# Kernel optimization log

Hardware: AMD Instinct MI355X
Metric: run time of the kernel (lower is better)

The kernel has to match this reference:

```python
import jax, jax.numpy as jnp
import numpy as np
import math

B, T, C, H = 2, 2048, 1024, 16
HD = C // H  # head dim = 64

def setup_inputs() -> dict:
    key = jax.random.key(0)
    ks = jax.random.split(key, 5)
    s = 1.0 / math.sqrt(C)
    return {
        "x": jax.random.normal(ks[0], (B, T, C), jnp.float32),
        "Wq": jax.random.normal(ks[1], (C, C), jnp.float32) * s,
        "bq": jnp.zeros((C,), jnp.float32),
        "Wk": jax.random.normal(ks[2], (C, C), jnp.float32) * s,
        "bk": jnp.zeros((C,), jnp.float32),
        "Wv": jax.random.normal(ks[3], (C, C), jnp.float32) * s,
        "bv": jnp.zeros((C,), jnp.float32),
        "Wp": jax.random.normal(ks[4], (C, C), jnp.float32) * s,
        "bp": jnp.zeros((C,), jnp.float32),
    }

def reference(x, Wq, bq, Wk, bk, Wv, bv, Wp, bp):
    # project and split heads: [B,T,C] -> [B,H,T,HD]
    def heads(y):
        return y.reshape(B, T, H, HD).transpose(0, 2, 1, 3)
    q = heads(x @ Wq + bq)
    k = heads(x @ Wk + bk)
    v = heads(x @ Wv + bv)
    scale = 1.0 / math.sqrt(HD)
    att = jnp.einsum('bhqd,bhkd->bhqk', q, k) * scale  # [B,H,T,T]
    causal = jnp.tril(jnp.ones((T, T), bool))
    att = jnp.where(causal, att, -jnp.inf)
    att = jax.nn.softmax(att, axis=-1)  # attention_dropout p=0 -> identity
    y = jnp.einsum('bhqk,bhkd->bhqd', att, v)  # [B,H,T,HD]
    y = y.transpose(0, 2, 1, 3).reshape(B, T, C)
    return y @ Wp + bp  # residual_dropout p=0 -> identity
```

## Files before the change

kernel.cpp:

```cpp
#include <hip/hip_runtime.h>
#include <hip/hip_bf16.h>
#include <stdint.h>

typedef __bf16 bf16x8 __attribute__((ext_vector_type(8)));
typedef __bf16 bf16x4 __attribute__((ext_vector_type(4)));
typedef float  f32x4  __attribute__((ext_vector_type(4)));

#define MFMA16(a, b, c) __builtin_amdgcn_mfma_f32_16x16x32_bf16(a, b, c, 0, 0, 0)

#if __has_builtin(__builtin_amdgcn_exp2f)
#define EXP2(x) __builtin_amdgcn_exp2f(x)
#else
#define EXP2(x) exp2f(x)
#endif

__device__ __forceinline__ void ld16(void* lds, const void* g) {
    __builtin_amdgcn_global_load_lds(
        (const __attribute__((address_space(1))) void*)(uintptr_t)g,
        (__attribute__((address_space(3))) void*)(uint32_t)(uintptr_t)lds,
        16, 0, 0);
}

__global__ __launch_bounds__(1024) void prep_kernel(const float* __restrict__ x,
                                                    const float* __restrict__ W0,
                                                    const float* __restrict__ W1,
                                                    const float* __restrict__ W2,
                                                    const float* __restrict__ W3,
                                                    __bf16* __restrict__ wdst,
                                                    __bf16* __restrict__ xdst) {
    __shared__ __bf16 t[32][33];
    const int z = blockIdx.z;
    const int tx = threadIdx.x, ty = threadIdx.y;
    if (z == 4) {
        int blin = blockIdx.y * 32 + blockIdx.x;
        int i = (blin * 1024 + ty * 32 + tx) * 4;
        float4 v = *(const float4*)(x + i);
        xdst[i]     = (__bf16)v.x;
        xdst[i + 1] = (__bf16)v.y;
        xdst[i + 2] = (__bf16)v.z;
        xdst[i + 3] = (__bf16)v.w;
        return;
    }
    const float* W = (z == 0) ? W0 : (z == 1) ? W1 : (z == 2) ? W2 : W3;
    __bf16* D = wdst + (size_t)z * 1048576;
    t[ty][tx] = (__bf16)W[(size_t)(blockIdx.y * 32 + ty) * 1024 + blockIdx.x * 32 + tx];
    __syncthreads();
    D[(size_t)(blockIdx.x * 32 + ty) * 1024 + blockIdx.y * 32 + tx] = t[tx][ty];
}

__device__ __forceinline__ void gemm_mainloop(const __bf16* __restrict__ A,
                                              const __bf16* __restrict__ BT,
                                              int K, __bf16* As, __bf16* Bs,
                                              f32x4 acc[4][4]) {
    const int tid  = threadIdx.x;
    const int lane = tid & 63;
    const int wid  = tid >> 6;
    const int quad = lane >> 4;
    const int l16  = lane & 15;
    const int wm   = wid >> 1;
    const int wn   = wid & 1;

    const int srow = wid * 16 + (lane >> 2);
    const int scol = (lane & 3) * 8;
    const int sdst = wid * 512 + lane * 8;

    auto stage = [&](int b, int k0) {
        ld16(As + b * 4096 + sdst,        A  + (size_t)srow        * K + k0 + scol);
        ld16(As + b * 4096 + 2048 + sdst, A  + (size_t)(srow + 64) * K + k0 + scol);
        ld16(Bs + b * 4096 + sdst,        BT + (size_t)srow        * K + k0 + scol);
        ld16(Bs + b * 4096 + 2048 + sdst, BT + (size_t)(srow + 64) * K + k0 + scol);
    };

    stage(0, 0);
    __syncthreads();
    int buf = 0;

    for (int k0 = 0; k0 < K; k0 += 32) {
        if (k0 + 32 < K) stage(buf ^ 1, k0 + 32);
        bf16x8 af[4], bf[4];
#pragma unroll
        for (int mt = 0; mt < 4; mt++)
            af[mt] = *(const bf16x8*)(As + buf * 4096 +
                                      (wm * 64 + mt * 16 + l16) * 32 + quad * 8);
#pragma unroll
        for (int nt = 0; nt < 4; nt++)
            bf[nt] = *(const bf16x8*)(Bs + buf * 4096 +
                                      (wn * 64 + nt * 16 + l16) * 32 + quad * 8);
#pragma unroll
        for (int mt = 0; mt < 4; mt++)
#pragma unroll
            for (int nt = 0; nt < 4; nt++)
                acc[mt][nt] = MFMA16(af[mt], bf[nt], acc[mt][nt]);
        __syncthreads();
        buf ^= 1;
    }
}

__device__ __forceinline__ void mainloop64(const __bf16* __restrict__ A,
                                           const __bf16* __restrict__ BT,
                                           int K, __bf16* As, __bf16* Bs,
                                           f32x4 acc[2][4]) {
    const int tid  = threadIdx.x;
    const int lane = tid & 63;
    const int quad = lane >> 4;
    const int l16  = lane & 15;
    const int wid  = tid >> 6;
    const int wm   = wid >> 1;
    const int wn   = wid & 1;
    const int srow = tid >> 2;
    const int scol = (tid & 3) * 8;

    auto stage = [&](int b, int k0) {
        ld16(As + b * 2048 + tid * 8,        A  + (size_t)srow        * K + k0 + scol);
        ld16(Bs + b * 4096 + tid * 8,        BT + (size_t)srow        * K + k0 + scol);
        ld16(Bs + b * 4096 + 2048 + tid * 8, BT + (size_t)(srow + 64) * K + k0 + scol);
    };

    stage(0, 0);
    __syncthreads();
    int buf = 0;

    for (int k0 = 0; k0 < K; k0 += 32) {
        if (k0 + 32 < K) stage(buf ^ 1, k0 + 32);
        bf16x8 af[2], bf[4];
#pragma unroll
        for (int mt = 0; mt < 2; mt++)
            af[mt] = *(const bf16x8*)(As + buf * 2048 +
                                      (wm * 32 + mt * 16 + l16) * 32 + quad * 8);
#pragma unroll
        for (int nt = 0; nt < 4; nt++)
            bf[nt] = *(const bf16x8*)(Bs + buf * 4096 +
                                      (wn * 64 + nt * 16 + l16) * 32 + quad * 8);
#pragma unroll
        for (int mt = 0; mt < 2; mt++)
#pragma unroll
            for (int nt = 0; nt < 4; nt++)
                acc[mt][nt] = MFMA16(af[mt], bf[nt], acc[mt][nt]);
        __syncthreads();
        buf ^= 1;
    }
}

__global__ __launch_bounds__(256) void qkv_gemm(const __bf16* __restrict__ X,
                                                const __bf16* __restrict__ WTb,
                                                const float* __restrict__ b0,
                                                const float* __restrict__ b1,
                                                const float* __restrict__ b2,
                                                __bf16* __restrict__ qk,
                                                __bf16* __restrict__ vt) {
    __shared__ __attribute__((aligned(16))) __bf16 As[8192];
    __shared__ __attribute__((aligned(16))) __bf16 Bs[8192];
    const int o  = blockIdx.x;
    const int g  = o & 7, r = o >> 3;
    const int mB = ((g >> 1) << 3) + (r & 7);
    const int nz = (g & 1) * 12 + (r >> 3);
    const int z  = nz >> 3;
    const int n  = nz & 7;
    const __bf16* BT   = WTb + (size_t)z * 1048576;
    const float* bias  = (z == 0) ? b0 : (z == 1) ? b1 : b2;
    const int m0 = mB * 128, n0 = n * 128;
    f32x4 acc[4][4];
    const f32x4 zz = {0.f, 0.f, 0.f, 0.f};
#pragma unroll
    for (int i = 0; i < 4; i++)
#pragma unroll
        for (int j = 0; j < 4; j++) acc[i][j] = zz;
    gemm_mainloop(X + (size_t)m0 * 1024, BT + (size_t)n0 * 1024, 1024, As, Bs, acc);

    const int lane = threadIdx.x & 63, wid = threadIdx.x >> 6;
    const int quad = lane >> 4, l16 = lane & 15, wm = wid >> 1, wn = wid & 1;
    if (z == 2) {
#pragma unroll
        for (int nt = 0; nt < 4; nt++) {
            int col = n0 + wn * 64 + nt * 16 + l16;
            float bv = bias[col];
            int h = col >> 6, hd = col & 63;
#pragma unroll
            for (int mt = 0; mt < 4; mt++) {
                int m = m0 + wm * 64 + mt * 16 + quad * 4;
                int b = m >> 11, tt = m & 2047;
                bf16x4 pk;
                pk.x = (__bf16)(acc[mt][nt].x + bv);
                pk.y = (__bf16)(acc[mt][nt].y + bv);
                pk.z = (__bf16)(acc[mt][nt].z + bv);
                pk.w = (__bf16)(acc[mt][nt].w + bv);
                *(bf16x4*)(vt + ((size_t)((b * 16 + h) * 64 + hd)) * 2048 + tt) = pk;
            }
        }
    } else {
        const float sq = (z == 0) ? 0.18033688011112042f : 1.0f;
        __bf16* dst = qk + (size_t)z * 4194304;
#pragma unroll
        for (int nt = 0; nt < 4; nt++) {
            int col = n0 + wn * 64 + nt * 16 + l16;
            float bv = bias[col];
            int h = col >> 6, hd = col & 63;
#pragma unroll
            for (int mt = 0; mt < 4; mt++) {
#pragma unroll
                for (int r4 = 0; r4 < 4; r4++) {
                    int m = m0 + wm * 64 + mt * 16 + quad * 4 + r4;
                    int b = m >> 11, tt = m & 2047;
                    float v = (acc[mt][nt][r4] + bv) * sq;
                    dst[((size_t)((b * 16 + h) * 2048 + tt)) * 64 + hd] = (__bf16)v;
                }
            }
        }
    }
}

__global__ __launch_bounds__(256) void proj_gemm(const __bf16* __restrict__ Yw,
                                                 const __bf16* __restrict__ WT,
                                                 const float* __restrict__ bias,
                                                 float* __restrict__ out) {
    __shared__ __attribute__((aligned(16))) __bf16 As[4096];
    __shared__ __attribute__((aligned(16))) __bf16 Bs[8192];
    const int o = blockIdx.x;
    const int g = o & 7, r = o >> 3;
    const int m0 = (g * 8 + (r & 7)) * 64;
    const int n0 = (r >> 3) * 128;
    f32x4 acc[2][4];
    const f32x4 zz = {0.f, 0.f, 0.f, 0.f};
#pragma unroll
    for (int i = 0; i < 2; i++)
#pragma unroll
        for (int j = 0; j < 4; j++) acc[i][j] = zz;
    mainloop64(Yw + (size_t)m0 * 1024, WT + (size_t)n0 * 1024, 1024, As, Bs, acc);

    const int lane = threadIdx.x & 63, wid = threadIdx.x >> 6;
    const int quad = lane >> 4, l16 = lane & 15, wm = wid >> 1, wn = wid & 1;
#pragma unroll
    for (int nt = 0; nt < 4; nt++) {
        int col = n0 + wn * 64 + nt * 16 + l16;
        float bv = bias[col];
#pragma unroll
        for (int mt = 0; mt < 2; mt++) {
#pragma unroll
            for (int r4 = 0; r4 < 4; r4++) {
                int m = m0 + wm * 32 + mt * 16 + quad * 4 + r4;
                out[(size_t)m * 1024 + col] = acc[mt][nt][r4] + bv;
            }
        }
    }
}

__global__ __launch_bounds__(512, 1) void attn_kernel(const __bf16* __restrict__ Qg,
                                                      const __bf16* __restrict__ Kg,
                                                      const __bf16* __restrict__ Vtg,
                                                      __bf16* __restrict__ Y) {
    __shared__ __attribute__((aligned(16))) __bf16 Kb[2][128 * 64];
    __shared__ __attribute__((aligned(16))) __bf16 Vb[2][64 * 128];
    __shared__ __attribute__((aligned(16))) __bf16 Ps[8][16 * 136];
    __shared__ __attribute__((aligned(16))) float  Lw[8][16];

    const int tid  = threadIdx.x;
    const int lane = tid & 63;
    const int wid  = tid >> 6;
    const int quad = lane >> 4;
    const int l16  = lane & 15;
    const int bkid = blockIdx.x;
    const int head  = ((bkid & 7) << 2) + ((bkid >> 3) & 3);
    const int ipair = bkid >> 5;
    const size_t hbase = (size_t)head * (2048 * 64);
    const f32x4 zz = {0.f, 0.f, 0.f, 0.f};

    const int kr  = lane >> 3;
    const int kc8 = (lane & 7) ^ kr;
    const int vr  = lane >> 4;
    const int vl  = lane & 15;

#pragma unroll 1
    for (int itm = 0; itm < 2; itm++) {
        const int qi  = itm ? (15 - ipair) : ipair;
        const int ktl = qi;
        const int q0  = qi << 7;
        const int q0w = q0 + wid * 16;

        bf16x8 qf[2];
#pragma unroll
        for (int kk = 0; kk < 2; kk++)
            qf[kk] = *(const bf16x8*)(Qg + hbase +
                                      (size_t)(q0w + l16) * 64 + kk * 32 + quad * 8);

        f32x4 acc_o[4];
#pragma unroll
        for (int jj = 0; jj < 4; jj++) acc_o[jj] = zz;
        float l_s = 0.f;

        auto stage = [&](int bf, int key0) {
#pragma unroll
            for (int i = 0; i < 2; i++) {
                const int c = wid * 2 + i;
                ld16((char*)&Kb[bf][0] + c * 1024 + lane * 16,
                     Kg + hbase + (size_t)(key0 + c * 8 + kr) * 64 + kc8 * 8);
            }
#pragma unroll
            for (int i = 0; i < 2; i++) {
                const int c = wid * 2 + i;
                const int row = c * 4 + vr;
                const int vc  = vl ^ (row & 7);
                ld16((char*)&Vb[bf][0] + c * 1024 + lane * 16,
                     Vtg + hbase + (size_t)row * 2048 + key0 + vc * 8);
            }
        };

        stage(0, 0);
        __syncthreads();
        int buf = 0;

#pragma unroll 1
        for (int kt = 0; kt <= ktl; kt++) {
            if (kt < ktl) stage(buf ^ 1, (kt + 1) << 7);

            f32x4 accs[8];
#pragma unroll
            for (int mt = 0; mt < 8; mt++) accs[mt] = zz;
#pragma unroll
            for (int kk = 0; kk < 2; kk++) {
#pragma unroll
                for (int mt = 0; mt < 8; mt++) {
                    bf16x8 kf = *(const bf16x8*)(&Kb[buf][(mt * 16 + l16) * 64 +
                                                 (((kk * 4 + quad) ^ (l16 & 7)) << 3)]);
                    accs[mt] = MFMA16(kf, qf[kk], accs[mt]);
                }
            }

            if (kt == ktl) {
#pragma unroll
                for (int mt = 0; mt < 8; mt++) {
                    int q_g = wid * 16 + l16;
#pragma unroll
                    for (int r4 = 0; r4 < 4; r4++) {
                        int key_g = mt * 16 + quad * 4 + r4;
                        if (key_g > q_g) accs[mt][r4] = -1e30f;
                    }
                }
            }

            float s_s = 0.f;
#pragma unroll
            for (int mt = 0; mt < 8; mt++) {
                f32x4 pv;
                pv.x = EXP2(accs[mt].x);
                pv.y = EXP2(accs[mt].y);
                pv.z = EXP2(accs[mt].z);
                pv.w = EXP2(accs[mt].w);
                s_s += (pv.x + pv.y) + (pv.z + pv.w);
                bf16x4 pk;
                pk.x = (__bf16)pv.x; pk.y = (__bf16)pv.y;
                pk.z = (__bf16)pv.z; pk.w = (__bf16)pv.w;
                *(bf16x4*)(&Ps[wid][l16 * 136 + mt * 16 + quad * 4]) = pk;
            }
            {
                float t = s_s;
                t += __shfl_xor(t, 16);
                t += __shfl_xor(t, 32);
                l_s += t;
            }

#pragma unroll
            for (int kk = 0; kk < 4; kk++) {
                bf16x8 pf, vf[4];
                pf = *(const bf16x8*)(&Ps[wid][l16 * 136 + kk * 32 + quad * 8]);
#pragma unroll
                for (int nv = 0; nv < 4; nv++)
                    vf[nv] = *(const bf16x8*)(&Vb[buf][(nv * 16 + l16) * 128 +
                                              (((kk * 4 + quad) ^ (l16 & 7)) << 3)]);
#pragma unroll
                for (int nv = 0; nv < 4; nv++)
                    acc_o[nv] = MFMA16(pf, vf[nv], acc_o[nv]);
            }

            __syncthreads();
            buf ^= 1;
        }

        if (quad == 0) Lw[wid][l16] = l_s;
        float* Om = (float*)&Ps[wid][0];
#pragma unroll
        for (int nv = 0; nv < 4; nv++)
#pragma unroll
            for (int r4 = 0; r4 < 4; r4++)
                Om[(quad * 4 + r4) * 68 + nv * 16 + l16] = acc_o[nv][r4];
        __syncthreads();

        {
            const int q  = lane >> 2;
            const int d0 = (lane & 3) * 16;
            float li = 1.0f / Lw[wid][q];
            f32x4 s0 = *(const f32x4*)(&Om[q * 68 + d0]);
            f32x4 s1 = *(const f32x4*)(&Om[q * 68 + d0 + 4]);
            f32x4 s2 = *(const f32x4*)(&Om[q * 68 + d0 + 8]);
            f32x4 s3 = *(const f32x4*)(&Om[q * 68 + d0 + 12]);
            bf16x8 o0, o1;
            o0[0] = (__bf16)(s0.x * li); o0[1] = (__bf16)(s0.y * li);
            o0[2] = (__bf16)(s0.z * li); o0[3] = (__bf16)(s0.w * li);
            o0[4] = (__bf16)(s1.x * li); o0[5] = (__bf16)(s1.y * li);
            o0[6] = (__bf16)(s1.z * li); o0[7] = (__bf16)(s1.w * li);
            o1[0] = (__bf16)(s2.x * li); o1[1] = (__bf16)(s2.y * li);
            o1[2] = (__bf16)(s2.z * li); o1[3] = (__bf16)(s2.w * li);
            o1[4] = (__bf16)(s3.x * li); o1[5] = (__bf16)(s3.y * li);
            o1[6] = (__bf16)(s3.z * li); o1[7] = (__bf16)(s3.w * li);
            const int bb = head >> 4, hh = head & 15;
            __bf16* yp = Y + ((size_t)(bb * 2048 + q0w + q)) * 1024 + hh * 64 + d0;
            *(bf16x8*)(yp)     = o0;
            *(bf16x8*)(yp + 8) = o1;
        }
        __syncthreads();
    }
}

#define XB_OFF  0
#define WT_OFF  4194304
#define Q_OFF   8388608
#define K_OFF   12582912
#define VT_OFF  16777216
#define Y_OFF   0

extern "C" void kernel_launch(void* const* d_in, const int* in_sizes, int n_in,
                              void* d_out, int out_size, void* d_ws, size_t ws_size,
                              hipStream_t stream) {
    const float* x  = (const float*)d_in[0];
    const float* Wq = (const float*)d_in[1];
    const float* bq = (const float*)d_in[2];
    const float* Wk = (const float*)d_in[3];
    const float* bk = (const float*)d_in[4];
    const float* Wv = (const float*)d_in[5];
    const float* bv = (const float*)d_in[6];
    const float* Wp = (const float*)d_in[7];
    const float* bp = (const float*)d_in[8];
    __bf16* ws  = (__bf16*)d_ws;
    float*  out = (float*)d_out;
    if (ws_size < (size_t)41943040) return;

    prep_kernel<<<dim3(32, 32, 5), dim3(32, 32), 0, stream>>>(x, Wq, Wk, Wv, Wp,
                                                              ws + WT_OFF, ws + XB_OFF);
    qkv_gemm<<<dim3(768), 256, 0, stream>>>(ws + XB_OFF, ws + WT_OFF, bq, bk, bv,
                                            ws + Q_OFF, ws + VT_OFF);
    attn_kernel<<<dim3(256), 512, 0, stream>>>(ws + Q_OFF, ws + K_OFF, ws + VT_OFF,
                                               ws + Y_OFF);
    proj_gemm<<<dim3(512), 256, 0, stream>>>(ws + Y_OFF, ws + WT_OFF + 3 * 1048576, bp, out);
}
```

Baseline: 176.9 us.

## Split attention into one q-tile per block and run two blocks per CU

The attention kernel previously had 256 blocks. Each processed a balanced pair of q-tiles (qi and 15-qi) with double-buffered K/V tiles in LDS. Now it launches 512 blocks, each handling a single q-tile with single-buffered K/V. The launch bounds are raised to allow two blocks per CU, so a co-resident block hides load latency instead of software prefetch. This halves LDS per block, but it drops the explicit load/compute overlap, adds a sync stall per tile, and gives up the pairing that balanced causal work across blocks.

New measurement: 185.5 us. +4.8%, slower.

```diff
diff --git a/kernel.cpp b/kernel.cpp
--- a/kernel.cpp
+++ b/kernel.cpp
@@ -244,12 +244,12 @@
     }
 }
 
-__global__ __launch_bounds__(512, 1) void attn_kernel(const __bf16* __restrict__ Qg,
+__global__ __launch_bounds__(512, 2) void attn_kernel(const __bf16* __restrict__ Qg,
                                                       const __bf16* __restrict__ Kg,
                                                       const __bf16* __restrict__ Vtg,
                                                       __bf16* __restrict__ Y) {
-    __shared__ __attribute__((aligned(16))) __bf16 Kb[2][128 * 64];
-    __shared__ __attribute__((aligned(16))) __bf16 Vb[2][64 * 128];
+    __shared__ __attribute__((aligned(16))) __bf16 Kb[128 * 64];
+    __shared__ __attribute__((aligned(16))) __bf16 Vb[64 * 128];
     __shared__ __attribute__((aligned(16))) __bf16 Ps[8][16 * 136];
     __shared__ __attribute__((aligned(16))) float  Lw[8][16];
 
@@ -259,8 +259,10 @@
     const int quad = lane >> 4;
     const int l16  = lane & 15;
     const int bkid = blockIdx.x;
-    const int head  = ((bkid & 7) << 2) + ((bkid >> 3) & 3);
-    const int ipair = bkid >> 5;
+    const int head = ((bkid & 7) << 2) + ((bkid >> 3) & 3);
+    const int qi   = bkid >> 5;
+    const int ktl  = qi;
+    const int q0w  = (qi << 7) + wid * 16;
     const size_t hbase = (size_t)head * (2048 * 64);
     const f32x4 zz = {0.f, 0.f, 0.f, 0.f};
 
@@ -269,144 +271,132 @@
     const int vr  = lane >> 4;
     const int vl  = lane & 15;
 
+    bf16x8 qf[2];
+#pragma unroll
+    for (int kk = 0; kk < 2; kk++)
+        qf[kk] = *(const bf16x8*)(Qg + hbase +
+                                  (size_t)(q0w + l16) * 64 + kk * 32 + quad * 8);
+
+    f32x4 acc_o[4];
+#pragma unroll
+    for (int jj = 0; jj < 4; jj++) acc_o[jj] = zz;
+    float l_s = 0.f;
+
+    auto stage = [&](int key0) {
+#pragma unroll
+        for (int i = 0; i < 2; i++) {
+            const int c = wid * 2 + i;
+            ld16((char*)Kb + c * 1024 + lane * 16,
+                 Kg + hbase + (size_t)(key0 + c * 8 + kr) * 64 + kc8 * 8);
+        }
+#pragma unroll
+        for (int i = 0; i < 2; i++) {
+            const int c = wid * 2 + i;
+            const int row = c * 4 + vr;
+            const int vc  = vl ^ (row & 7);
+            ld16((char*)Vb + c * 1024 + lane * 16,
+                 Vtg + hbase + (size_t)row * 2048 + key0 + vc * 8);
+        }
+    };
+
 #pragma unroll 1
-    for (int itm = 0; itm < 2; itm++) {
-        const int qi  = itm ? (15 - ipair) : ipair;
-        const int ktl = qi;
-        const int q0  = qi << 7;
-        const int q0w = q0 + wid * 16;
-
-        bf16x8 qf[2];
-#pragma unroll
-        for (int kk = 0; kk < 2; kk++)
-            qf[kk] = *(const bf16x8*)(Qg + hbase +
-                                      (size_t)(q0w + l16) * 64 + kk * 32 + quad * 8);
-
-        f32x4 acc_o[4];
-#pragma unroll
-        for (int jj = 0; jj < 4; jj++) acc_o[jj] = zz;
-        float l_s = 0.f;
-
-        auto stage = [&](int bf, int key0) {
-#pragma unroll
-            for (int i = 0; i < 2; i++) {
-                const int c = wid * 2 + i;
-                ld16((char*)&Kb[bf][0] + c * 1024 + lane * 16,
-                     Kg + hbase + (size_t)(key0 + c * 8 + kr) * 64 + kc8 * 8);
+    for (int kt = 0; kt <= ktl; kt++) {
+        stage(kt << 7);
+        __syncthreads();
+
+        f32x4 accs[8];
+#pragma unroll
+        for (int mt = 0; mt < 8; mt++) accs[mt] = zz;
+#pragma unroll
+        for (int kk = 0; kk < 2; kk++) {
+#pragma unroll
+            for (int mt = 0; mt < 8; mt++) {
+                bf16x8 kf = *(const bf16x8*)(&Kb[(mt * 16 + l16) * 64 +
+                                             (((kk * 4 + quad) ^ (l16 & 7)) << 3)]);
+                accs[mt] = MFMA16(kf, qf[kk], accs[mt]);
             }
-#pragma unroll
-            for (int i = 0; i < 2; i++) {
-                const int c = wid * 2 + i;
-                const int row = c * 4 + vr;
-                const int vc  = vl ^ (row & 7);
-                ld16((char*)&Vb[bf][0] + c * 1024 + lane * 16,
-                     Vtg + hbase + (size_t)row * 2048 + key0 + vc * 8);
-            }
-        };
-
-        stage(0, 0);
-        __syncthreads();
-        int buf = 0;
-
-#pragma unroll 1
-        for (int kt = 0; kt <= ktl; kt++) {
-            if (kt < ktl) stage(buf ^ 1, (kt + 1) << 7);
-
-            f32x4 accs[8];
-#pragma unroll
-            for (int mt = 0; mt < 8; mt++) accs[mt] = zz;
-#pragma unroll
-            for (int kk = 0; kk < 2; kk++) {
-#pragma unroll
-                for (int mt = 0; mt < 8; mt++) {
-                    bf16x8 kf = *(const bf16x8*)(&Kb[buf][(mt * 16 + l16) * 64 +
-                                                 (((kk * 4 + quad) ^ (l16 & 7)) << 3)]);
-                    accs[mt] = MFMA16(kf, qf[kk], accs[mt]);
+        }
+
+        if (kt == ktl) {
+#pragma unroll
+            for (int mt = 0; mt < 8; mt++) {
+                int q_g = wid * 16 + l16;
+#pragma unroll
+                for (int r4 = 0; r4 < 4; r4++) {
+                    int key_g = mt * 16 + quad * 4 + r4;
+                    if (key_g > q_g) accs[mt][r4] = -1e30f;
                 }
             }
-
-            if (kt == ktl) {
-#pragma unroll
-                for (int mt = 0; mt < 8; mt++) {
-                    int q_g = wid * 16 + l16;
-#pragma unroll
-                    for (int r4 = 0; r4 < 4; r4++) {
-                        int key_g = mt * 16 + quad * 4 + r4;
-                        if (key_g > q_g) accs[mt][r4] = -1e30f;
-                    }
-                }
-            }
-
-            float s_s = 0.f;
-#pragma unroll
-            for (int mt = 0; mt < 8; mt++) {
-                f32x4 pv;
-                pv.x = EXP2(accs[mt].x);
-                pv.y = EXP2(accs[mt].y);
-                pv.z = EXP2(accs[mt].z);
-                pv.w = EXP2(accs[mt].w);
-                s_s += (pv.x + pv.y) + (pv.z + pv.w);
-                bf16x4 pk;
-                pk.x = (__bf16)pv.x; pk.y = (__bf16)pv.y;
-                pk.z = (__bf16)pv.z; pk.w = (__bf16)pv.w;
-                *(bf16x4*)(&Ps[wid][l16 * 136 + mt * 16 + quad * 4]) = pk;
-            }
-            {
-                float t = s_s;
-                t += __shfl_xor(t, 16);
-                t += __shfl_xor(t, 32);
-                l_s += t;
-            }
-
-#pragma unroll
-            for (int kk = 0; kk < 4; kk++) {
-                bf16x8 pf, vf[4];
-                pf = *(const bf16x8*)(&Ps[wid][l16 * 136 + kk * 32 + quad * 8]);
-#pragma unroll
-                for (int nv = 0; nv < 4; nv++)
-                    vf[nv] = *(const bf16x8*)(&Vb[buf][(nv * 16 + l16) * 128 +
-                                              (((kk * 4 + quad) ^ (l16 & 7)) << 3)]);
-#pragma unroll
-                for (int nv = 0; nv < 4; nv++)
-                    acc_o[nv] = MFMA16(pf, vf[nv], acc_o[nv]);
-            }
-
-            __syncthreads();
-            buf ^= 1;
-        }
-
-        if (quad == 0) Lw[wid][l16] = l_s;
-        float* Om = (float*)&Ps[wid][0];
-#pragma unroll
-        for (int nv = 0; nv < 4; nv++)
-#pragma unroll
-            for (int r4 = 0; r4 < 4; r4++)
-                Om[(quad * 4 + r4) * 68 + nv * 16 + l16] = acc_o[nv][r4];
+        }
+
+        float s_s = 0.f;
+#pragma unroll
+        for (int mt = 0; mt < 8; mt++) {
+            f32x4 pv;
+            pv.x = EXP2(accs[mt].x);
+            pv.y = EXP2(accs[mt].y);
+            pv.z = EXP2(accs[mt].z);
+            pv.w = EXP2(accs[mt].w);
+            s_s += (pv.x + pv.y) + (pv.z + pv.w);
+            bf16x4 pk;
+            pk.x = (__bf16)pv.x; pk.y = (__bf16)pv.y;
+            pk.z = (__bf16)pv.z; pk.w = (__bf16)pv.w;
+            *(bf16x4*)(&Ps[wid][l16 * 136 + mt * 16 + quad * 4]) = pk;
+        }
+        {
+            float t = s_s;
+            t += __shfl_xor(t, 16);
+            t += __shfl_xor(t, 32);
+            l_s += t;
+        }
+
+#pragma unroll
+        for (int kk = 0; kk < 4; kk++) {
+            bf16x8 pf, vf[4];
+            pf = *(const bf16x8*)(&Ps[wid][l16 * 136 + kk * 32 + quad * 8]);
+#pragma unroll
+            for (int nv = 0; nv < 4; nv++)
+                vf[nv] = *(const bf16x8*)(&Vb[(nv * 16 + l16) * 128 +
+                                          (((kk * 4 + quad) ^ (l16 & 7)) << 3)]);
+#pragma unroll
+            for (int nv = 0; nv < 4; nv++)
+                acc_o[nv] = MFMA16(pf, vf[nv], acc_o[nv]);
+        }
+
         __syncthreads();
-
-        {
-            const int q  = lane >> 2;
-            const int d0 = (lane & 3) * 16;
-            float li = 1.0f / Lw[wid][q];
-            f32x4 s0 = *(const f32x4*)(&Om[q * 68 + d0]);
-            f32x4 s1 = *(const f32x4*)(&Om[q * 68 + d0 + 4]);
-            f32x4 s2 = *(const f32x4*)(&Om[q * 68 + d0 + 8]);
-            f32x4 s3 = *(const f32x4*)(&Om[q * 68 + d0 + 12]);
-            bf16x8 o0, o1;
-            o0[0] = (__bf16)(s0.x * li); o0[1] = (__bf16)(s0.y * li);
-            o0[2] = (__bf16)(s0.z * li); o0[3] = (__bf16)(s0.w * li);
-            o0[4] = (__bf16)(s1.x * li); o0[5] = (__bf16)(s1.y * li);
-            o0[6] = (__bf16)(s1.z * li); o0[7] = (__bf16)(s1.w * li);
-            o1[0] = (__bf16)(s2.x * li); o1[1] = (__bf16)(s2.y * li);
-            o1[2] = (__bf16)(s2.z * li); o1[3] = (__bf16)(s2.w * li);
-            o1[4] = (__bf16)(s3.x * li); o1[5] = (__bf16)(s3.y * li);
-            o1[6] = (__bf16)(s3.z * li); o1[7] = (__bf16)(s3.w * li);
-            const int bb = head >> 4, hh = head & 15;
-            __bf16* yp = Y + ((size_t)(bb * 2048 + q0w + q)) * 1024 + hh * 64 + d0;
-            *(bf16x8*)(yp)     = o0;
-            *(bf16x8*)(yp + 8) = o1;
-        }
-        __syncthreads();
+    }
+
+    if (quad == 0) Lw[wid][l16] = l_s;
+    float* Om = (float*)&Ps[wid][0];
+#pragma unroll
+    for (int nv = 0; nv < 4; nv++)
+#pragma unroll
+        for (int r4 = 0; r4 < 4; r4++)
+            Om[(quad * 4 + r4) * 68 + nv * 16 + l16] = acc_o[nv][r4];
+    __syncthreads();
+
+    {
+        const int q  = lane >> 2;
+        const int d0 = (lane & 3) * 16;
+        float li = 1.0f / Lw[wid][q];
+        f32x4 s0 = *(const f32x4*)(&Om[q * 68 + d0]);
+        f32x4 s1 = *(const f32x4*)(&Om[q * 68 + d0 + 4]);
+        f32x4 s2 = *(const f32x4*)(&Om[q * 68 + d0 + 8]);
+        f32x4 s3 = *(const f32x4*)(&Om[q * 68 + d0 + 12]);
+        bf16x8 o0, o1;
+        o0[0] = (__bf16)(s0.x * li); o0[1] = (__bf16)(s0.y * li);
+        o0[2] = (__bf16)(s0.z * li); o0[3] = (__bf16)(s0.w * li);
+        o0[4] = (__bf16)(s1.x * li); o0[5] = (__bf16)(s1.y * li);
+        o0[6] = (__bf16)(s1.z * li); o0[7] = (__bf16)(s1.w * li);
+        o1[0] = (__bf16)(s2.x * li); o1[1] = (__bf16)(s2.y * li);
+        o1[2] = (__bf16)(s2.z * li); o1[3] = (__bf16)(s2.w * li);
+        o1[4] = (__bf16)(s3.x * li); o1[5] = (__bf16)(s3.y * li);
+        o1[6] = (__bf16)(s3.z * li); o1[7] = (__bf16)(s3.w * li);
+        const int bb = head >> 4, hh = head & 15;
+        __bf16* yp = Y + ((size_t)(bb * 2048 + (qi << 7) + wid * 16 + q)) * 1024 +
+                     hh * 64 + d0;
+        *(bf16x8*)(yp)     = o0;
+        *(bf16x8*)(yp + 8) = o1;
     }
 }
 
@@ -437,7 +427,7 @@
                                                               ws + WT_OFF, ws + XB_OFF);
     qkv_gemm<<<dim3(768), 256, 0, stream>>>(ws + XB_OFF, ws + WT_OFF, bq, bk, bv,
                                             ws + Q_OFF, ws + VT_OFF);
-    attn_kernel<<<dim3(256), 512, 0, stream>>>(ws + Q_OFF, ws + K_OFF, ws + VT_OFF,
+    attn_kernel<<<dim3(512), 512, 0, stream>>>(ws + Q_OFF, ws + K_OFF, ws + VT_OFF,
                                                ws + Y_OFF);
     proj_gemm<<<dim3(512), 256, 0, stream>>>(ws + Y_OFF, ws + WT_OFF + 3 * 1048576, bp, out);
 }
```
